# Performance work log

Measured on AMD Instinct MI355X. Metric: run time of the kernel, lower is better.

## Reference

```python
import jax, jax.numpy as jnp
import numpy as np

B, L, C, H, WS = 8, 1024, 1024, 16, 128  # batch, seq (grid 32x32), dim, heads, window_size
HD = C // H


def _local_mask(seq_len, window_size):
    # blocked where |i - j| > window_size // 2 (matches create_local_attention_mask)
    idx = jnp.arange(seq_len)
    return jnp.abs(idx[:, None] - idx[None, :]) > window_size // 2  # True = blocked


def setup_inputs() -> dict:
    key = jax.random.key(0)
    k0, k1, k2 = jax.random.split(key, 3)
    x = jax.random.normal(k0, (B, L, C), jnp.float32)
    in_proj_w = jax.random.normal(k1, (3 * C, C), jnp.float32) * 0.02
    in_proj_b = jnp.zeros((3 * C,), jnp.float32)
    out_w = jax.random.normal(k2, (C, C), jnp.float32) * 0.02
    out_b = jnp.zeros((C,), jnp.float32)
    return {"x": x, "in_proj_w": in_proj_w, "in_proj_b": in_proj_b,
            "out_w": out_w, "out_b": out_b}


def reference(x, in_proj_w, in_proj_b, out_w, out_b):
    # nn.MultiheadAttention (batch_first, self-attention) with boolean attn_mask.
    Bc, Lc, Cc = x.shape
    qkv = x @ in_proj_w.T + in_proj_b              # [B, L, 3C]
    q, k, v = jnp.split(qkv, 3, axis=-1)
    to_heads = lambda t: t.reshape(Bc, Lc, H, HD).transpose(0, 2, 1, 3)  # [B,H,L,hd]
    q, k, v = to_heads(q), to_heads(k), to_heads(v)
    scale = 1.0 / np.sqrt(HD).astype(np.float32)
    scores = jnp.einsum('bhqd,bhkd->bhqk', q, k) * scale  # [B,H,L,L]
    blocked = _local_mask(Lc, WS)
    scores = jnp.where(blocked[None, None], -jnp.inf, scores)
    attn = jax.nn.softmax(scores, axis=-1)
    out = jnp.einsum('bhqk,bhkd->bhqd', attn, v)           # [B,H,L,hd]
    out = out.transpose(0, 2, 1, 3).reshape(Bc, Lc, Cc)
    return out @ out_w.T + out_b
```

## Files before the change

kernel.cpp:

```cpp
#include <hip/hip_runtime.h>
#include <hip/hip_bf16.h>
#include <stdint.h>


typedef __attribute__((ext_vector_type(8))) short bf16x8;
typedef __attribute__((ext_vector_type(4))) float f32x4;

__device__ inline unsigned short f2b(float f) {
    __hip_bfloat16 h = __float2bfloat16(f);
    return *reinterpret_cast<unsigned short*>(&h);
}

__device__ inline void gld16(const unsigned short* g, unsigned short* l) {
    __builtin_amdgcn_global_load_lds(
        (const __attribute__((address_space(1))) void*)g,
        (__attribute__((address_space(3))) void*)l, 16, 0, 0);
}

#define BM 128
#define BN 128
#define BK 64

__global__ void __launch_bounds__(256) cast_inputs(
    const float4* __restrict__ x, const float4* __restrict__ w1,
    const float4* __restrict__ w2,
    uint2* __restrict__ xb, uint2* __restrict__ w1b, uint2* __restrict__ w2b)
{
    const int N0 = 2097152, N1 = 786432, N2 = 262144;
    int stride = gridDim.x * blockDim.x;
    for (int i = blockIdx.x * blockDim.x + threadIdx.x; i < N0 + N1 + N2; i += stride) {
        const float4* src; uint2* dst; int idx;
        if (i < N0)            { src = x;  dst = xb;  idx = i; }
        else if (i < N0 + N1)  { src = w1; dst = w1b; idx = i - N0; }
        else                   { src = w2; dst = w2b; idx = i - N0 - N1; }
        float4 f = src[idx];
        unsigned short t[4] = {f2b(f.x), f2b(f.y), f2b(f.z), f2b(f.w)};
        dst[idx] = *(uint2*)t;
    }
}

__global__ void __launch_bounds__(256) gemm_qkv(
    const unsigned short* __restrict__ A,
    const unsigned short* __restrict__ W,
    const float* __restrict__ bias,
    unsigned short* __restrict__ Qo,
    unsigned short* __restrict__ Ko,
    unsigned short* __restrict__ Vo)
{
    const int K = 1024;
    int n0 = blockIdx.x * BN;
    int m0 = blockIdx.y * BM;
    int tid = threadIdx.x;
    int wave = tid >> 6, lane = tid & 63;
    int lm = lane & 15, quad = lane >> 4;
    int mblk = (wave & 1) * 64, nblk = (wave >> 1) * 64;

    __shared__ unsigned short As[BM * BK];
    __shared__ unsigned short Bs[BN * BK];

    int drow = lane >> 3;
    int gcc  = (lane & 7) ^ drow;
    const unsigned short* ga[4]; const unsigned short* gb[4];
    unsigned short *la[4], *lb[4];
#pragma unroll
    for (int p = 0; p < 4; ++p) {
        int r = wave * 32 + p * 8 + drow;
        ga[p] = A + (size_t)(m0 + r) * K + gcc * 8;
        gb[p] = W + (size_t)(n0 + r) * K + gcc * 8;
        la[p] = As + (wave * 32 + p * 8) * 64;
        lb[p] = Bs + (wave * 32 + p * 8) * 64;
    }
    int lm7 = lm & 7;

    f32x4 acc[4][4];
#pragma unroll
    for (int i = 0; i < 4; ++i)
#pragma unroll
        for (int j = 0; j < 4; ++j)
            acc[i][j] = (f32x4){0.f, 0.f, 0.f, 0.f};

    for (int k0 = 0; k0 < K; k0 += BK) {
        __syncthreads();
#pragma unroll
        for (int p = 0; p < 4; ++p) gld16(ga[p] + k0, la[p]);
#pragma unroll
        for (int p = 0; p < 4; ++p) gld16(gb[p] + k0, lb[p]);
        __syncthreads();
        bf16x8 af[4][2], bfr[4][2];
#pragma unroll
        for (int i = 0; i < 4; ++i)
#pragma unroll
            for (int hhh = 0; hhh < 2; ++hhh)
                af[i][hhh] = *(const bf16x8*)(As + (mblk + i * 16 + lm) * 64 +
                                              (((hhh * 4 + quad) ^ lm7) << 3));
#pragma unroll
        for (int j = 0; j < 4; ++j)
#pragma unroll
            for (int hhh = 0; hhh < 2; ++hhh)
                bfr[j][hhh] = *(const bf16x8*)(Bs + (nblk + j * 16 + lm) * 64 +
                                               (((hhh * 4 + quad) ^ lm7) << 3));
#pragma unroll
        for (int i = 0; i < 4; ++i)
#pragma unroll
            for (int j = 0; j < 4; ++j) {
                acc[i][j] = __builtin_amdgcn_mfma_f32_16x16x32_bf16(af[i][0], bfr[j][0], acc[i][j], 0, 0, 0);
                acc[i][j] = __builtin_amdgcn_mfma_f32_16x16x32_bf16(af[i][1], bfr[j][1], acc[i][j], 0, 0, 0);
            }
    }

#pragma unroll
    for (int j = 0; j < 4; ++j) {
        int n = n0 + nblk + j * 16 + lm;
        float bv = bias[n];
        int sec = n >> 10, rem = n & 1023;
        int h = rem >> 6, d = rem & 63;
        unsigned short* dst = (sec == 0) ? Qo : (sec == 1) ? Ko : Vo;
#pragma unroll
        for (int i = 0; i < 4; ++i) {
#pragma unroll
            for (int r = 0; r < 4; ++r) {
                int m = m0 + mblk + i * 16 + quad * 4 + r;
                int bb = m >> 10, sl = m & 1023;
                size_t idx = ((size_t)((bb * 16 + h) * 1024 + sl)) * 64 + d;
                dst[idx] = f2b(acc[i][j][r] + bv);
            }
        }
    }
}

__global__ void __launch_bounds__(256) attn_local(
    const unsigned short* __restrict__ Qg,
    const unsigned short* __restrict__ Kg,
    const unsigned short* __restrict__ Vg,
    unsigned short* __restrict__ Og)
{
    const int KP = 72;
    const int VP = 200;
    __shared__ unsigned short Ks[192 * KP];
    __shared__ unsigned short Vt[64 * VP];

    int tid = threadIdx.x;
    int wave = tid >> 6, lane = tid & 63;
    int lm = lane & 15, quad = lane >> 4;

    int bh = blockIdx.x >> 4;
    int qt = blockIdx.x & 15;
    int q0 = qt * 64;
    int b = bh >> 4, h = bh & 15;
    const unsigned short* Qbh = Qg + (size_t)bh * 1024 * 64;
    const unsigned short* Kbh = Kg + (size_t)bh * 1024 * 64;
    const unsigned short* Vbh = Vg + (size_t)bh * 1024 * 64;
    int j0 = q0 - 64;

#pragma unroll
    for (int it = 0; it < 6; ++it) {
        int id = it * 256 + tid;
        int r = id >> 3;
        int c = (id & 7) * 8;
        int j = j0 + r;
        uint4 kv, vv;
        kv.x = kv.y = kv.z = kv.w = 0;
        vv = kv;
        if (j >= 0 && j < 1024) {
            kv = *(const uint4*)(Kbh + (size_t)j * 64 + c);
            vv = *(const uint4*)(Vbh + (size_t)j * 64 + c);
        }
        *(uint4*)(Ks + r * KP + c) = kv;
        unsigned short tmp[8];
        *(uint4*)tmp = vv;
#pragma unroll
        for (int e = 0; e < 8; ++e) Vt[(c + e) * VP + r] = tmp[e];
    }
    __syncthreads();

    int qrow = q0 + wave * 16;
    bf16x8 qf0 = *(const bf16x8*)(Qbh + (size_t)(qrow + lm) * 64 + quad * 8);
    bf16x8 qf1 = *(const bf16x8*)(Qbh + (size_t)(qrow + lm) * 64 + 32 + quad * 8);

    f32x4 sc[12];
#pragma unroll
    for (int kt = 0; kt < 12; ++kt) {
        f32x4 a = (f32x4){0.f, 0.f, 0.f, 0.f};
        bf16x8 k0f = *(const bf16x8*)(Ks + (kt * 16 + lm) * KP + quad * 8);
        bf16x8 k1f = *(const bf16x8*)(Ks + (kt * 16 + lm) * KP + 32 + quad * 8);
        a = __builtin_amdgcn_mfma_f32_16x16x32_bf16(qf0, k0f, a, 0, 0, 0);
        a = __builtin_amdgcn_mfma_f32_16x16x32_bf16(qf1, k1f, a, 0, 0, 0);
        sc[kt] = a;
    }

    float mx[4] = {-3e38f, -3e38f, -3e38f, -3e38f};
#pragma unroll
    for (int kt = 0; kt < 12; ++kt) {
        int jg = j0 + kt * 16 + lm;
#pragma unroll
        for (int r = 0; r < 4; ++r) {
            int irow = q0 + wave * 16 + quad * 4 + r;
            int diff = irow - jg;
            bool ok = (jg >= 0) && (jg < 1024) && (diff <= 64) && (diff >= -64);
            float s = ok ? sc[kt][r] * 0.125f : -30000.0f;
            sc[kt][r] = s;
            mx[r] = fmaxf(mx[r], s);
        }
    }
#pragma unroll
    for (int off = 1; off <= 8; off <<= 1)
#pragma unroll
        for (int r = 0; r < 4; ++r)
            mx[r] = fmaxf(mx[r], __shfl_xor(mx[r], off, 64));

    float sum[4] = {0.f, 0.f, 0.f, 0.f};
#pragma unroll
    for (int kt = 0; kt < 12; ++kt)
#pragma unroll
        for (int r = 0; r < 4; ++r) {
            float p = __expf(sc[kt][r] - mx[r]);
            sc[kt][r] = p;
            sum[r] += p;
        }
#pragma unroll
    for (int off = 1; off <= 8; off <<= 1)
#pragma unroll
        for (int r = 0; r < 4; ++r)
            sum[r] += __shfl_xor(sum[r], off, 64);

    __syncthreads();
    unsigned short* Pb = Ks + wave * 3200;
#pragma unroll
    for (int kt = 0; kt < 12; ++kt)
#pragma unroll
        for (int r = 0; r < 4; ++r)
            Pb[(quad * 4 + r) * VP + kt * 16 + lm] = f2b(sc[kt][r]);
    __syncthreads();

    f32x4 o[4];
#pragma unroll
    for (int n = 0; n < 4; ++n) o[n] = (f32x4){0.f, 0.f, 0.f, 0.f};
#pragma unroll
    for (int jc = 0; jc < 6; ++jc) {
        bf16x8 pf = *(const bf16x8*)(Pb + lm * VP + jc * 32 + quad * 8);
#pragma unroll
        for (int n = 0; n < 4; ++n) {
            bf16x8 vf = *(const bf16x8*)(Vt + (n * 16 + lm) * VP + jc * 32 + quad * 8);
            o[n] = __builtin_amdgcn_mfma_f32_16x16x32_bf16(pf, vf, o[n], 0, 0, 0);
        }
    }

    float inv[4];
#pragma unroll
    for (int r = 0; r < 4; ++r) inv[r] = 1.0f / sum[r];
#pragma unroll
    for (int n = 0; n < 4; ++n)
#pragma unroll
        for (int r = 0; r < 4; ++r) {
            int orow = q0 + wave * 16 + quad * 4 + r;
            size_t oidx = ((size_t)(b * 1024 + orow)) * 1024 + h * 64 + n * 16 + lm;
            Og[oidx] = f2b(o[n][r] * inv[r]);
        }
}

__global__ void __launch_bounds__(256) gemm_proj(
    const unsigned short* __restrict__ A,
    const unsigned short* __restrict__ W,
    const float* __restrict__ bias,
    float* __restrict__ Out)
{
    const int K = 1024;
    int n0 = blockIdx.x * BN;
    int m0 = blockIdx.y * BM;
    int tid = threadIdx.x;
    int wave = tid >> 6, lane = tid & 63;
    int lm = lane & 15, quad = lane >> 4;
    int mblk = (wave & 1) * 64, nblk = (wave >> 1) * 64;

    __shared__ unsigned short As[BM * BK];
    __shared__ unsigned short Bs[BN * BK];

    int drow = lane >> 3;
    int gcc  = (lane & 7) ^ drow;
    const unsigned short* ga[4]; const unsigned short* gb[4];
    unsigned short *la[4], *lb[4];
#pragma unroll
    for (int p = 0; p < 4; ++p) {
        int r = wave * 32 + p * 8 + drow;
        ga[p] = A + (size_t)(m0 + r) * K + gcc * 8;
        gb[p] = W + (size_t)(n0 + r) * K + gcc * 8;
        la[p] = As + (wave * 32 + p * 8) * 64;
        lb[p] = Bs + (wave * 32 + p * 8) * 64;
    }
    int lm7 = lm & 7;

    f32x4 acc[4][4];
#pragma unroll
    for (int i = 0; i < 4; ++i)
#pragma unroll
        for (int j = 0; j < 4; ++j)
            acc[i][j] = (f32x4){0.f, 0.f, 0.f, 0.f};

    for (int k0 = 0; k0 < K; k0 += BK) {
        __syncthreads();
#pragma unroll
        for (int p = 0; p < 4; ++p) gld16(ga[p] + k0, la[p]);
#pragma unroll
        for (int p = 0; p < 4; ++p) gld16(gb[p] + k0, lb[p]);
        __syncthreads();
        bf16x8 af[4][2], bfr[4][2];
#pragma unroll
        for (int i = 0; i < 4; ++i)
#pragma unroll
            for (int hhh = 0; hhh < 2; ++hhh)
                af[i][hhh] = *(const bf16x8*)(As + (mblk + i * 16 + lm) * 64 +
                                              (((hhh * 4 + quad) ^ lm7) << 3));
#pragma unroll
        for (int j = 0; j < 4; ++j)
#pragma unroll
            for (int hhh = 0; hhh < 2; ++hhh)
                bfr[j][hhh] = *(const bf16x8*)(Bs + (nblk + j * 16 + lm) * 64 +
                                               (((hhh * 4 + quad) ^ lm7) << 3));
#pragma unroll
        for (int i = 0; i < 4; ++i)
#pragma unroll
            for (int j = 0; j < 4; ++j) {
                acc[i][j] = __builtin_amdgcn_mfma_f32_16x16x32_bf16(af[i][0], bfr[j][0], acc[i][j], 0, 0, 0);
                acc[i][j] = __builtin_amdgcn_mfma_f32_16x16x32_bf16(af[i][1], bfr[j][1], acc[i][j], 0, 0, 0);
            }
    }

#pragma unroll
    for (int j = 0; j < 4; ++j) {
        int n = n0 + nblk + j * 16 + lm;
        float bv = bias[n];
#pragma unroll
        for (int i = 0; i < 4; ++i) {
#pragma unroll
            for (int r = 0; r < 4; ++r) {
                int m = m0 + mblk + i * 16 + quad * 4 + r;
                Out[(size_t)m * 1024 + n] = acc[i][j][r] + bv;
            }
        }
    }
}

extern "C" void kernel_launch(void* const* d_in, const int* in_sizes, int n_in,
                              void* d_out, int out_size, void* d_ws, size_t ws_size,
                              hipStream_t stream) {
    const float* x  = (const float*)d_in[0];
    const float* w1 = (const float*)d_in[1];
    const float* b1 = (const float*)d_in[2];
    const float* w2 = (const float*)d_in[3];
    const float* b2 = (const float*)d_in[4];
    float* out = (float*)d_out;

    char* ws = (char*)d_ws;
    const size_t MB = 1024 * 1024;
    unsigned short* xb   = (unsigned short*)(ws);
    unsigned short* w1b  = (unsigned short*)(ws + 16 * MB);
    unsigned short* w2b  = (unsigned short*)(ws + 22 * MB);
    unsigned short* q    = (unsigned short*)(ws + 24 * MB);
    unsigned short* k    = (unsigned short*)(ws + 40 * MB);
    unsigned short* v    = (unsigned short*)d_out;
    unsigned short* attn = (unsigned short*)(ws);

    dim3 blk(256);
    cast_inputs<<<3072, blk, 0, stream>>>(
        (const float4*)x, (const float4*)w1, (const float4*)w2,
        (uint2*)xb, (uint2*)w1b, (uint2*)w2b);
    gemm_qkv<<<dim3(24, 64), blk, 0, stream>>>(xb, w1b, b1, q, k, v);
    attn_local<<<dim3(2048), blk, 0, stream>>>(q, k, v, attn);
    gemm_proj<<<dim3(8, 64), blk, 0, stream>>>(attn, w2b, b2, out);
}
```

Baseline: 210.8 us.

## Store V transposed from QKV GEMM and skip fully masked key tiles per wave

The QKV projection epilogue now writes V in [bh, d, seq] layout, so the attention kernel can load V^T with vectorized 16-byte reads instead of scattering scalar LDS stores to transpose it. Each wave now computes scores only for the 9 key tiles that can intersect its 16-row band (of 12), and runs 5 instead of 6 PV chunks, zeroing the one unused 16-column tile in its P buffer. The V epilogue store becomes strided across sequence, which may hurt write coalescing in the GEMM. The V load also relies on 8-aligned boundaries for the edge check.

After: 238.5 us. 1.13x slower.

```diff
diff --git a/kernel.cpp b/kernel.cpp
--- a/kernel.cpp
+++ b/kernel.cpp
@@ -114,15 +114,20 @@
         float bv = bias[n];
         int sec = n >> 10, rem = n & 1023;
         int h = rem >> 6, d = rem & 63;
-        unsigned short* dst = (sec == 0) ? Qo : (sec == 1) ? Ko : Vo;
 #pragma unroll
         for (int i = 0; i < 4; ++i) {
 #pragma unroll
             for (int r = 0; r < 4; ++r) {
                 int m = m0 + mblk + i * 16 + quad * 4 + r;
                 int bb = m >> 10, sl = m & 1023;
-                size_t idx = ((size_t)((bb * 16 + h) * 1024 + sl)) * 64 + d;
-                dst[idx] = f2b(acc[i][j][r] + bv);
+                int bh = bb * 16 + h;
+                unsigned short val = f2b(acc[i][j][r] + bv);
+                if (sec == 0)
+                    Qo[((size_t)bh * 1024 + sl) * 64 + d] = val;
+                else if (sec == 1)
+                    Ko[((size_t)bh * 1024 + sl) * 64 + d] = val;
+                else
+                    Vo[((size_t)bh * 64 + d) * 1024 + sl] = val;
             }
         }
     }
@@ -149,7 +154,7 @@
     int b = bh >> 4, h = bh & 15;
     const unsigned short* Qbh = Qg + (size_t)bh * 1024 * 64;
     const unsigned short* Kbh = Kg + (size_t)bh * 1024 * 64;
-    const unsigned short* Vbh = Vg + (size_t)bh * 1024 * 64;
+    const unsigned short* Vbh = Vg + (size_t)bh * 64 * 1024;
     int j0 = q0 - 64;
 
 #pragma unroll
@@ -158,18 +163,19 @@
         int r = id >> 3;
         int c = (id & 7) * 8;
         int j = j0 + r;
-        uint4 kv, vv;
-        kv.x = kv.y = kv.z = kv.w = 0;
-        vv = kv;
-        if (j >= 0 && j < 1024) {
-            kv = *(const uint4*)(Kbh + (size_t)j * 64 + c);
-            vv = *(const uint4*)(Vbh + (size_t)j * 64 + c);
-        }
+        uint4 kv; kv.x = kv.y = kv.z = kv.w = 0;
+        if (j >= 0 && j < 1024) kv = *(const uint4*)(Kbh + (size_t)j * 64 + c);
         *(uint4*)(Ks + r * KP + c) = kv;
-        unsigned short tmp[8];
-        *(uint4*)tmp = vv;
-#pragma unroll
-        for (int e = 0; e < 8; ++e) Vt[(c + e) * VP + r] = tmp[e];
+    }
+#pragma unroll
+    for (int it = 0; it < 6; ++it) {
+        int id = it * 256 + tid;
+        int d = id / 24;
+        int c = id - d * 24;
+        int j = j0 + c * 8;
+        uint4 vv; vv.x = vv.y = vv.z = vv.w = 0;
+        if (j >= 0 && j + 7 < 1024) vv = *(const uint4*)(Vbh + (size_t)d * 1024 + j);
+        *(uint4*)(Vt + d * VP + c * 8) = vv;
     }
     __syncthreads();
 
@@ -177,12 +183,13 @@
     bf16x8 qf0 = *(const bf16x8*)(Qbh + (size_t)(qrow + lm) * 64 + quad * 8);
     bf16x8 qf1 = *(const bf16x8*)(Qbh + (size_t)(qrow + lm) * 64 + 32 + quad * 8);
 
-    f32x4 sc[12];
-#pragma unroll
-    for (int kt = 0; kt < 12; ++kt) {
+    f32x4 sc[9];
+#pragma unroll
+    for (int kt = 0; kt < 9; ++kt) {
+        int akt = wave + kt;
         f32x4 a = (f32x4){0.f, 0.f, 0.f, 0.f};
-        bf16x8 k0f = *(const bf16x8*)(Ks + (kt * 16 + lm) * KP + quad * 8);
-        bf16x8 k1f = *(const bf16x8*)(Ks + (kt * 16 + lm) * KP + 32 + quad * 8);
+        bf16x8 k0f = *(const bf16x8*)(Ks + (akt * 16 + lm) * KP + quad * 8);
+        bf16x8 k1f = *(const bf16x8*)(Ks + (akt * 16 + lm) * KP + 32 + quad * 8);
         a = __builtin_amdgcn_mfma_f32_16x16x32_bf16(qf0, k0f, a, 0, 0, 0);
         a = __builtin_amdgcn_mfma_f32_16x16x32_bf16(qf1, k1f, a, 0, 0, 0);
         sc[kt] = a;
@@ -190,8 +197,8 @@
 
     float mx[4] = {-3e38f, -3e38f, -3e38f, -3e38f};
 #pragma unroll
-    for (int kt = 0; kt < 12; ++kt) {
-        int jg = j0 + kt * 16 + lm;
+    for (int kt = 0; kt < 9; ++kt) {
+        int jg = j0 + (wave + kt) * 16 + lm;
 #pragma unroll
         for (int r = 0; r < 4; ++r) {
             int irow = q0 + wave * 16 + quad * 4 + r;
@@ -210,7 +217,7 @@
 
     float sum[4] = {0.f, 0.f, 0.f, 0.f};
 #pragma unroll
-    for (int kt = 0; kt < 12; ++kt)
+    for (int kt = 0; kt < 9; ++kt)
 #pragma unroll
         for (int r = 0; r < 4; ++r) {
             float p = __expf(sc[kt][r] - mx[r]);
@@ -226,17 +233,27 @@
     __syncthreads();
     unsigned short* Pb = Ks + wave * 3200;
 #pragma unroll
-    for (int kt = 0; kt < 12; ++kt)
+    for (int kt = 0; kt < 9; ++kt) {
+        int akt = wave + kt;
 #pragma unroll
         for (int r = 0; r < 4; ++r)
-            Pb[(quad * 4 + r) * VP + kt * 16 + lm] = f2b(sc[kt][r]);
+            Pb[(quad * 4 + r) * VP + akt * 16 + lm] = f2b(sc[kt][r]);
+    }
+    {
+        int zkt = (wave & 1) ? (wave - 1) : (wave + 9);
+#pragma unroll
+        for (int r = 0; r < 4; ++r)
+            Pb[(quad * 4 + r) * VP + zkt * 16 + lm] = 0;
+    }
     __syncthreads();
 
+    int jclo = wave >> 1;
     f32x4 o[4];
 #pragma unroll
     for (int n = 0; n < 4; ++n) o[n] = (f32x4){0.f, 0.f, 0.f, 0.f};
 #pragma unroll
-    for (int jc = 0; jc < 6; ++jc) {
+    for (int jc2 = 0; jc2 < 5; ++jc2) {
+        int jc = jclo + jc2;
         bf16x8 pf = *(const bf16x8*)(Pb + lm * VP + jc * 32 + quad * 8);
 #pragma unroll
         for (int n = 0; n < 4; ++n) {
```
